# Optimization experiments

Measured on AMD Instinct MI355X. Metric: run time of the kernel, lower is better.

Reference implementation:

```python
import jax, jax.numpy as jnp
import numpy as np

WINDOW_SIZE = 100  # band half-width = WINDOW_SIZE // 2 = 50, inclusive


def setup_inputs() -> dict:
    key = jax.random.key(0)
    kq, kk, kv = jax.random.split(key, 3)
    shape = (2, 8, 4096, 64)  # [B, H, S, D]
    return {
        "query": jax.random.normal(kq, shape, dtype=jnp.float32),
        "key": jax.random.normal(kk, shape, dtype=jnp.float32),
        "value": jax.random.normal(kv, shape, dtype=jnp.float32),
    }


def reference(query, key, value):
    B, H, S, D = query.shape
    half = WINDOW_SIZE // 2
    scale = 1.0 / jnp.sqrt(jnp.asarray(D, dtype=jnp.float32))
    # Full dense scores (faithful to the original module): [B, H, S, S]
    scores = jnp.einsum("bhqd,bhkd->bhqk", query, key) * scale
    # Sliding-window band mask: row i attends to j in [i-half, i+half]
    idx = jnp.arange(S)
    band = jnp.abs(idx[:, None] - idx[None, :]) <= half  # [S, S]
    scores = jnp.where(band[None, None, :, :], scores, -jnp.inf)
    attn = jax.nn.softmax(scores, axis=-1)
    attn = jnp.nan_to_num(attn, nan=0.0)  # matches torch.nan_to_num(w, 0.0)
    return jnp.einsum("bhqk,bhkd->bhqd", attn, value)
```

## Files before the change

### kernel.cpp

```cpp
#include <hip/hip_runtime.h>

#define S_LEN 4096
#define DIM   64
#define HALF  50
#define RB    256
#define WQ    16
#define THREADS 1024
#define KCAP  384
#define SCALE 0.125f

typedef __attribute__((ext_vector_type(8))) short bf16x8;
typedef __attribute__((ext_vector_type(4))) float f32x4;

__device__ __forceinline__ unsigned int bf16_rne(float f) {
    unsigned int u = __float_as_uint(f);
    return (u + 0x7fffu + ((u >> 16) & 1u)) >> 16;
}
__device__ __forceinline__ unsigned int pk2(float lo, float hi) {
    return bf16_rne(lo) | (bf16_rne(hi) << 16);
}

__global__ __launch_bounds__(THREADS)
void lattn_mfma(const float* __restrict__ Q, const float* __restrict__ K,
                const float* __restrict__ V, float* __restrict__ O) {
    __shared__ unsigned short Ks[KCAP * 64];
    __shared__ unsigned short Vs[DIM * KCAP];
    __shared__ unsigned short Ps[16 * 16 * 40];

    const int nwg = gridDim.x;
    const int cpx = nwg >> 3;
    const int bid = blockIdx.x;
    const int logical = (bid & 7) * cpx + (bid >> 3);
    const int bh = logical >> 4;
    const int r0 = (logical & 15) * RB;

    const size_t base = (size_t)bh * (S_LEN * DIM);
    const float* Qg = Q + base;
    const float* Kg = K + base;
    const float* Vg = V + base;
    float*       Og = O + base;

    const int kstart = (r0 >= HALF) ? ((r0 - HALF) & ~31) : 0;
    const int kend   = min(S_LEN, r0 + RB + HALF);
    const int nstep  = (kend - kstart + 31) >> 5;
    const int nkeys  = nstep << 5;

    const int u = threadIdx.x;

    for (int idx = u; idx < (nkeys << 3); idx += THREADS) {
        const int krow = idx >> 3;
        const int oct  = idx & 7;
        const int kg   = kstart + krow;
        unsigned int w0, w1, w2, w3;
        if (kg < kend) {
            const float4 a = *(const float4*)(Kg + (size_t)kg * DIM + oct * 8);
            const float4 b = *(const float4*)(Kg + (size_t)kg * DIM + oct * 8 + 4);
            w0 = pk2(a.x, a.y); w1 = pk2(a.z, a.w);
            w2 = pk2(b.x, b.y); w3 = pk2(b.z, b.w);
        } else { w0 = w1 = w2 = w3 = 0u; }
        *(uint4*)(Ks + krow * 64 + ((oct ^ (krow & 7)) << 3)) = make_uint4(w0, w1, w2, w3);
    }

    for (int idx = u; idx < (nkeys << 2); idx += THREADS) {
        const int kp = idx >> 3;
        const int m  = idx & 7;
        const int d0 = m * 8;
        const int k0 = kp * 2;
        const int kg = kstart + k0;
        unsigned int pw[8];
        if (kg < kend) {
            const float* va = Vg + (size_t)kg * DIM + d0;
            const float* vb = va + DIM;
            float a0[8], a1[8];
            *(float4*)a0 = *(const float4*)va;  *(float4*)(a0 + 4) = *(const float4*)(va + 4);
            *(float4*)a1 = *(const float4*)vb;  *(float4*)(a1 + 4) = *(const float4*)(vb + 4);
            #pragma unroll
            for (int j = 0; j < 8; ++j) pw[j] = pk2(a0[j], a1[j]);
        } else {
            #pragma unroll
            for (int j = 0; j < 8; ++j) pw[j] = 0u;
        }
        #pragma unroll
        for (int j = 0; j < 8; ++j) {
            const int jj = (j + m) & 7;
            const int d  = d0 + jj;
            const int sl = (k0 >> 3) ^ (d & 7);
            *(unsigned int*)(Vs + d * KCAP + sl * 8 + (k0 & 7)) = pw[jj];
        }
    }

    const int lane = u & 63;
    const int wv_  = u >> 6;
    const int g  = lane >> 4;
    const int cc = lane & 15;
    const int qlo = r0 + WQ * wv_;

    bf16x8 qf[2];
    #pragma unroll
    for (int ds = 0; ds < 2; ++ds) {
        const float* src = Qg + (size_t)(qlo + cc) * DIM + ds * 32 + g * 8;
        const float4 a = *(const float4*)src;
        const float4 b = *(const float4*)(src + 4);
        uint4 t = make_uint4(pk2(a.x * SCALE, a.y * SCALE), pk2(a.z * SCALE, a.w * SCALE),
                             pk2(b.x * SCALE, b.y * SCALE), pk2(b.z * SCALE, b.w * SCALE));
        qf[ds] = __builtin_bit_cast(bf16x8, t);
    }

    __syncthreads();

    f32x4 oacc[4] = {};
    float denom = 0.f;

    int lo = (qlo >= HALF) ? (qlo - HALF) : 0;
    lo = max(kstart, lo & ~31);
    const int t0 = (lo - kstart) >> 5;
    const int hi = min(kend, qlo + WQ - 1 + HALF + 1);
    const int t1 = (hi - kstart + 31) >> 5;

    unsigned short* Pw = Ps + wv_ * (16 * 40);

    for (int st = t0; st < t1; ++st) {
        const int kb = st << 5;

        f32x4 sacc[2] = {};
        #pragma unroll
        for (int ds = 0; ds < 2; ++ds) {
            #pragma unroll
            for (int kt = 0; kt < 2; ++kt) {
                const int krow = kb + kt * 16 + cc;
                const int sl   = (ds * 4 + g) ^ (krow & 7);
                const bf16x8 ka = *(const bf16x8*)(Ks + krow * 64 + sl * 8);
                sacc[kt] = __builtin_amdgcn_mfma_f32_16x16x32_bf16(ka, qf[ds], sacc[kt], 0, 0, 0);
            }
        }

        const int q = qlo + cc;
        #pragma unroll
        for (int kt = 0; kt < 2; ++kt) {
            float w4[4];
            const int keyb = kstart + kb + kt * 16 + g * 4;
            #pragma unroll
            for (int r = 0; r < 4; ++r) {
                const int key = keyb + r;
                const float e = __expf(sacc[kt][r]);
                const int dd  = key - q;
                const bool ok = (dd >= -HALF) && (dd <= HALF) && (key < S_LEN);
                w4[r] = ok ? e : 0.f;
                denom += w4[r];
            }
            *(uint2*)(Pw + cc * 40 + kt * 16 + g * 4) = make_uint2(pk2(w4[0], w4[1]), pk2(w4[2], w4[3]));
        }

        const bf16x8 pf = *(const bf16x8*)(Pw + cc * 40 + g * 8);
        #pragma unroll
        for (int dt = 0; dt < 4; ++dt) {
            const int d  = dt * 16 + cc;
            const int sl = ((kb >> 3) + g) ^ (d & 7);
            const bf16x8 vf = *(const bf16x8*)(Vs + d * KCAP + sl * 8);
            oacc[dt] = __builtin_amdgcn_mfma_f32_16x16x32_bf16(vf, pf, oacc[dt], 0, 0, 0);
        }
    }

    denom += __shfl_xor(denom, 16);
    denom += __shfl_xor(denom, 32);
    const float rinv = 1.f / denom;
    float* dst = Og + (size_t)(qlo + cc) * DIM;
    #pragma unroll
    for (int dt = 0; dt < 4; ++dt) {
        const f32x4 o = oacc[dt];
        *(float4*)(dst + dt * 16 + g * 4) =
            make_float4(o[0] * rinv, o[1] * rinv, o[2] * rinv, o[3] * rinv);
    }
}

extern "C" void kernel_launch(void* const* d_in, const int* in_sizes, int n_in,
                              void* d_out, int out_size, void* d_ws, size_t ws_size,
                              hipStream_t stream) {
    const float* q = (const float*)d_in[0];
    const float* k = (const float*)d_in[1];
    const float* v = (const float*)d_in[2];
    float* o = (float*)d_out;
    const int nbh = in_sizes[0] / (S_LEN * DIM);
    dim3 grid((S_LEN / RB) * nbh);
    lattn_mfma<<<grid, THREADS, 0, stream>>>(q, k, v, o);
}
```

Before: 21.84 us.

## Stream K/V into shared memory in chunks, prefetching the next chunk during compute

Replaces the up-front load of all K and V rows into shared memory with three 128-key chunks. The next chunk's global loads are issued into registers before computing on the current chunk, then converted, written to shared memory and followed by a barrier. This is meant to hide global-memory latency behind MFMA work, since each CU runs only one large block. It costs extra barriers and registers, and also clamps the exponent argument to 60 before exp.

```diff
diff --git a/kernel.cpp b/kernel.cpp
--- a/kernel.cpp
+++ b/kernel.cpp
@@ -7,6 +7,8 @@
 #define WQ    16
 #define THREADS 1024
 #define KCAP  384
+#define CHUNK 128
+#define NCH   3
 #define SCALE 0.125f
 
 typedef __attribute__((ext_vector_type(8))) short bf16x8;
@@ -42,51 +44,59 @@
 
     const int kstart = (r0 >= HALF) ? ((r0 - HALF) & ~31) : 0;
     const int kend   = min(S_LEN, r0 + RB + HALF);
-    const int nstep  = (kend - kstart + 31) >> 5;
-    const int nkeys  = nstep << 5;
+    const int nkeys  = ((kend - kstart + 31) >> 5) << 5;
 
     const int u = threadIdx.x;
 
-    for (int idx = u; idx < (nkeys << 3); idx += THREADS) {
-        const int krow = idx >> 3;
-        const int oct  = idx & 7;
-        const int kg   = kstart + krow;
-        unsigned int w0, w1, w2, w3;
+    auto k_load = [&](int c, float4& a, float4& b) {
+        const int kg  = kstart + c * CHUNK + (u >> 3);
+        const int oct = u & 7;
         if (kg < kend) {
-            const float4 a = *(const float4*)(Kg + (size_t)kg * DIM + oct * 8);
-            const float4 b = *(const float4*)(Kg + (size_t)kg * DIM + oct * 8 + 4);
-            w0 = pk2(a.x, a.y); w1 = pk2(a.z, a.w);
-            w2 = pk2(b.x, b.y); w3 = pk2(b.z, b.w);
-        } else { w0 = w1 = w2 = w3 = 0u; }
-        *(uint4*)(Ks + krow * 64 + ((oct ^ (krow & 7)) << 3)) = make_uint4(w0, w1, w2, w3);
-    }
-
-    for (int idx = u; idx < (nkeys << 2); idx += THREADS) {
-        const int kp = idx >> 3;
-        const int m  = idx & 7;
-        const int d0 = m * 8;
-        const int k0 = kp * 2;
-        const int kg = kstart + k0;
-        unsigned int pw[8];
-        if (kg < kend) {
-            const float* va = Vg + (size_t)kg * DIM + d0;
-            const float* vb = va + DIM;
-            float a0[8], a1[8];
-            *(float4*)a0 = *(const float4*)va;  *(float4*)(a0 + 4) = *(const float4*)(va + 4);
-            *(float4*)a1 = *(const float4*)vb;  *(float4*)(a1 + 4) = *(const float4*)(vb + 4);
-            #pragma unroll
-            for (int j = 0; j < 8; ++j) pw[j] = pk2(a0[j], a1[j]);
+            a = *(const float4*)(Kg + (size_t)kg * DIM + oct * 8);
+            b = *(const float4*)(Kg + (size_t)kg * DIM + oct * 8 + 4);
         } else {
-            #pragma unroll
-            for (int j = 0; j < 8; ++j) pw[j] = 0u;
-        }
-        #pragma unroll
-        for (int j = 0; j < 8; ++j) {
-            const int jj = (j + m) & 7;
-            const int d  = d0 + jj;
-            const int sl = (k0 >> 3) ^ (d & 7);
-            *(unsigned int*)(Vs + d * KCAP + sl * 8 + (k0 & 7)) = pw[jj];
-        }
+            a = make_float4(0.f, 0.f, 0.f, 0.f); b = a;
+        }
+    };
+    auto k_write = [&](int c, float4 a, float4 b) {
+        const int krow = c * CHUNK + (u >> 3);
+        const int oct  = u & 7;
+        *(uint4*)(Ks + krow * 64 + ((oct ^ (krow & 7)) << 3)) =
+            make_uint4(pk2(a.x, a.y), pk2(a.z, a.w), pk2(b.x, b.y), pk2(b.z, b.w));
+    };
+    auto v_load = [&](int c, float4* r) {
+        if (u < 512) {
+            const int kg = kstart + c * CHUNK + (u >> 3) * 2;
+            const int d0 = (u & 7) * 8;
+            if (kg < kend) {
+                const float* va = Vg + (size_t)kg * DIM + d0;
+                r[0] = *(const float4*)va;       r[1] = *(const float4*)(va + 4);
+                r[2] = *(const float4*)(va + DIM); r[3] = *(const float4*)(va + DIM + 4);
+            } else {
+                r[0] = make_float4(0.f, 0.f, 0.f, 0.f); r[1] = r[0]; r[2] = r[0]; r[3] = r[0];
+            }
+        }
+    };
+    auto v_write = [&](int c, const float4* r) {
+        if (u < 512) {
+            const int k0 = c * CHUNK + (u >> 3) * 2;
+            const int m  = u & 7;
+            const float* a0 = (const float*)r;
+            const float* a1 = (const float*)(r + 2);
+            #pragma unroll
+            for (int j = 0; j < 8; ++j) {
+                const int jj = (j + m) & 7;
+                const int d  = m * 8 + jj;
+                const int sl = (k0 >> 3) ^ (d & 7);
+                *(unsigned int*)(Vs + d * KCAP + sl * 8 + (k0 & 7)) = pk2(a0[jj], a1[jj]);
+            }
+        }
+    };
+
+    {
+        float4 ka, kb, vr[4];
+        k_load(0, ka, kb); v_load(0, vr);
+        k_write(0, ka, kb); v_write(0, vr);
     }
 
     const int lane = u & 63;
@@ -119,45 +129,60 @@
 
     unsigned short* Pw = Ps + wv_ * (16 * 40);
 
-    for (int st = t0; st < t1; ++st) {
-        const int kb = st << 5;
-
-        f32x4 sacc[2] = {};
-        #pragma unroll
-        for (int ds = 0; ds < 2; ++ds) {
+    for (int c = 0; c < NCH; ++c) {
+        float4 ka, kb, vr[4];
+        const bool more = (c + 1 < NCH) && ((c + 1) * CHUNK < nkeys);
+        if (more) { k_load(c + 1, ka, kb); v_load(c + 1, vr); }
+
+        const int sa = max(t0, c * 4);
+        const int sb = min(t1, c * 4 + 4);
+        for (int st = sa; st < sb; ++st) {
+            const int kb32 = st << 5;
+
+            f32x4 sacc[2] = {};
+            #pragma unroll
+            for (int ds = 0; ds < 2; ++ds) {
+                #pragma unroll
+                for (int kt = 0; kt < 2; ++kt) {
+                    const int krow = kb32 + kt * 16 + cc;
+                    const int sl   = (ds * 4 + g) ^ (krow & 7);
+                    const bf16x8 kfr = *(const bf16x8*)(Ks + krow * 64 + sl * 8);
+                    sacc[kt] = __builtin_amdgcn_mfma_f32_16x16x32_bf16(kfr, qf[ds], sacc[kt], 0, 0, 0);
+                }
+            }
+
+            const int q = qlo + cc;
             #pragma unroll
             for (int kt = 0; kt < 2; ++kt) {
-                const int krow = kb + kt * 16 + cc;
-                const int sl   = (ds * 4 + g) ^ (krow & 7);
-                const bf16x8 ka = *(const bf16x8*)(Ks + krow * 64 + sl * 8);
-                sacc[kt] = __builtin_amdgcn_mfma_f32_16x16x32_bf16(ka, qf[ds], sacc[kt], 0, 0, 0);
-            }
-        }
-
-        const int q = qlo + cc;
-        #pragma unroll
-        for (int kt = 0; kt < 2; ++kt) {
-            float w4[4];
-            const int keyb = kstart + kb + kt * 16 + g * 4;
-            #pragma unroll
-            for (int r = 0; r < 4; ++r) {
-                const int key = keyb + r;
-                const float e = __expf(sacc[kt][r]);
-                const int dd  = key - q;
-                const bool ok = (dd >= -HALF) && (dd <= HALF) && (key < S_LEN);
-                w4[r] = ok ? e : 0.f;
-                denom += w4[r];
-            }
-            *(uint2*)(Pw + cc * 40 + kt * 16 + g * 4) = make_uint2(pk2(w4[0], w4[1]), pk2(w4[2], w4[3]));
-        }
-
-        const bf16x8 pf = *(const bf16x8*)(Pw + cc * 40 + g * 8);
-        #pragma unroll
-        for (int dt = 0; dt < 4; ++dt) {
-            const int d  = dt * 16 + cc;
-            const int sl = ((kb >> 3) + g) ^ (d & 7);
-            const bf16x8 vf = *(const bf16x8*)(Vs + d * KCAP + sl * 8);
-            oacc[dt] = __builtin_amdgcn_mfma_f32_16x16x32_bf16(vf, pf, oacc[dt], 0, 0, 0);
+                float w4[4];
+                const int keyb = kstart + kb32 + kt * 16 + g * 4;
+                #pragma unroll
+                for (int r = 0; r < 4; ++r) {
+                    const int key = keyb + r;
+                    const float e = __expf(fminf(sacc[kt][r], 60.f));
+                    const int dd  = key - q;
+                    const bool ok = (dd >= -HALF) && (dd <= HALF) && (key < S_LEN);
+                    w4[r] = ok ? e : 0.f;
+                    denom += w4[r];
+                }
+                *(uint2*)(Pw + cc * 40 + kt * 16 + g * 4) =
+                    make_uint2(pk2(w4[0], w4[1]), pk2(w4[2], w4[3]));
+            }
+
+            const bf16x8 pf = *(const bf16x8*)(Pw + cc * 40 + g * 8);
+            #pragma unroll
+            for (int dt = 0; dt < 4; ++dt) {
+                const int d  = dt * 16 + cc;
+                const int sl = ((kb32 >> 3) + g) ^ (d & 7);
+                const bf16x8 vf = *(const bf16x8*)(Vs + d * KCAP + sl * 8);
+                oacc[dt] = __builtin_amdgcn_mfma_f32_16x16x32_bf16(vf, pf, oacc[dt], 0, 0, 0);
+            }
+        }
+
+        if (more) {
+            k_write(c + 1, ka, kb);
+            v_write(c + 1, vr);
+            __syncthreads();
         }
     }
 
```

After: 30.67 us. 1.4x slower.

## Load K directly from global per wave and overlap QK^T with V staging

Applied to the files above, without the earlier changes.

Removes the shared-memory K staging buffer: each wave reads its K rows straight from global memory, converts them to bf16 in registers and computes scores and probabilities for up to NT key tiles before the block barrier. This lets the QK^T/softmax work overlap with the cooperative V-to-LDS transpose, and the smaller LDS footprint plus launch_bounds(…,4) aims to raise occupancy. The V layout gets an extra XOR swizzle term to cut bank conflicts, and exp inputs are clamped at 60. The cost is redundant global K reads across waves (served mostly by cache) and extra registers to hold the buffered P fragments.

```diff
diff --git a/kernel.cpp b/kernel.cpp
--- a/kernel.cpp
+++ b/kernel.cpp
@@ -7,6 +7,7 @@
 #define WQ    16
 #define THREADS 1024
 #define KCAP  384
+#define NT    5
 #define SCALE 0.125f
 
 typedef __attribute__((ext_vector_type(8))) short bf16x8;
@@ -19,11 +20,14 @@
 __device__ __forceinline__ unsigned int pk2(float lo, float hi) {
     return bf16_rne(lo) | (bf16_rne(hi) << 16);
 }
+__device__ __forceinline__ bf16x8 cvt8(float4 a, float4 b) {
+    uint4 t = make_uint4(pk2(a.x, a.y), pk2(a.z, a.w), pk2(b.x, b.y), pk2(b.z, b.w));
+    return __builtin_bit_cast(bf16x8, t);
+}
 
-__global__ __launch_bounds__(THREADS)
+__global__ __launch_bounds__(THREADS, 4)
 void lattn_mfma(const float* __restrict__ Q, const float* __restrict__ K,
                 const float* __restrict__ V, float* __restrict__ O) {
-    __shared__ unsigned short Ks[KCAP * 64];
     __shared__ unsigned short Vs[DIM * KCAP];
     __shared__ unsigned short Ps[16 * 16 * 40];
 
@@ -42,24 +46,14 @@
 
     const int kstart = (r0 >= HALF) ? ((r0 - HALF) & ~31) : 0;
     const int kend   = min(S_LEN, r0 + RB + HALF);
-    const int nstep  = (kend - kstart + 31) >> 5;
-    const int nkeys  = nstep << 5;
+    const int nkeys  = ((kend - kstart + 31) >> 5) << 5;
 
     const int u = threadIdx.x;
-
-    for (int idx = u; idx < (nkeys << 3); idx += THREADS) {
-        const int krow = idx >> 3;
-        const int oct  = idx & 7;
-        const int kg   = kstart + krow;
-        unsigned int w0, w1, w2, w3;
-        if (kg < kend) {
-            const float4 a = *(const float4*)(Kg + (size_t)kg * DIM + oct * 8);
-            const float4 b = *(const float4*)(Kg + (size_t)kg * DIM + oct * 8 + 4);
-            w0 = pk2(a.x, a.y); w1 = pk2(a.z, a.w);
-            w2 = pk2(b.x, b.y); w3 = pk2(b.z, b.w);
-        } else { w0 = w1 = w2 = w3 = 0u; }
-        *(uint4*)(Ks + krow * 64 + ((oct ^ (krow & 7)) << 3)) = make_uint4(w0, w1, w2, w3);
-    }
+    const int lane = u & 63;
+    const int wv_  = u >> 6;
+    const int g  = lane >> 4;
+    const int cc = lane & 15;
+    const int qlo = r0 + WQ * wv_;
 
     for (int idx = u; idx < (nkeys << 2); idx += THREADS) {
         const int kp = idx >> 3;
@@ -67,49 +61,33 @@
         const int d0 = m * 8;
         const int k0 = kp * 2;
         const int kg = kstart + k0;
-        unsigned int pw[8];
+        float a0[8], a1[8];
         if (kg < kend) {
             const float* va = Vg + (size_t)kg * DIM + d0;
-            const float* vb = va + DIM;
-            float a0[8], a1[8];
-            *(float4*)a0 = *(const float4*)va;  *(float4*)(a0 + 4) = *(const float4*)(va + 4);
-            *(float4*)a1 = *(const float4*)vb;  *(float4*)(a1 + 4) = *(const float4*)(vb + 4);
-            #pragma unroll
-            for (int j = 0; j < 8; ++j) pw[j] = pk2(a0[j], a1[j]);
+            *(float4*)a0 = *(const float4*)va;        *(float4*)(a0 + 4) = *(const float4*)(va + 4);
+            *(float4*)a1 = *(const float4*)(va + DIM); *(float4*)(a1 + 4) = *(const float4*)(va + DIM + 4);
         } else {
             #pragma unroll
-            for (int j = 0; j < 8; ++j) pw[j] = 0u;
+            for (int j = 0; j < 8; ++j) { a0[j] = 0.f; a1[j] = 0.f; }
         }
         #pragma unroll
         for (int j = 0; j < 8; ++j) {
-            const int jj = (j + m) & 7;
-            const int d  = d0 + jj;
-            const int sl = (k0 >> 3) ^ (d & 7);
-            *(unsigned int*)(Vs + d * KCAP + sl * 8 + (k0 & 7)) = pw[jj];
+            const int d  = d0 + j;
+            const int sl = (k0 >> 3) ^ (d & 7) ^ ((d >> 3) & 7);
+            *(unsigned int*)(Vs + d * KCAP + sl * 8 + (k0 & 7)) = pk2(a0[j], a1[j]);
         }
     }
-
-    const int lane = u & 63;
-    const int wv_  = u >> 6;
-    const int g  = lane >> 4;
-    const int cc = lane & 15;
-    const int qlo = r0 + WQ * wv_;
 
     bf16x8 qf[2];
     #pragma unroll
     for (int ds = 0; ds < 2; ++ds) {
         const float* src = Qg + (size_t)(qlo + cc) * DIM + ds * 32 + g * 8;
-        const float4 a = *(const float4*)src;
-        const float4 b = *(const float4*)(src + 4);
-        uint4 t = make_uint4(pk2(a.x * SCALE, a.y * SCALE), pk2(a.z * SCALE, a.w * SCALE),
-                             pk2(b.x * SCALE, b.y * SCALE), pk2(b.z * SCALE, b.w * SCALE));
-        qf[ds] = __builtin_bit_cast(bf16x8, t);
+        float4 a = *(const float4*)src;
+        float4 b = *(const float4*)(src + 4);
+        a.x *= SCALE; a.y *= SCALE; a.z *= SCALE; a.w *= SCALE;
+        b.x *= SCALE; b.y *= SCALE; b.z *= SCALE; b.w *= SCALE;
+        qf[ds] = cvt8(a, b);
     }
-
-    __syncthreads();
-
-    f32x4 oacc[4] = {};
-    float denom = 0.f;
 
     int lo = (qlo >= HALF) ? (qlo - HALF) : 0;
     lo = max(kstart, lo & ~31);
@@ -118,46 +96,78 @@
     const int t1 = (hi - kstart + 31) >> 5;
 
     unsigned short* Pw = Ps + wv_ * (16 * 40);
+    float denom = 0.f;
+    bf16x8 pfr[NT];
 
-    for (int st = t0; st < t1; ++st) {
-        const int kb = st << 5;
+    #pragma unroll
+    for (int i = 0; i < NT; ++i) {
+        const int st = t0 + i;
+        if (st < t1) {
+            const int kb32 = st << 5;
 
-        f32x4 sacc[2] = {};
-        #pragma unroll
-        for (int ds = 0; ds < 2; ++ds) {
+            bf16x8 ka[2][2];
             #pragma unroll
             for (int kt = 0; kt < 2; ++kt) {
-                const int krow = kb + kt * 16 + cc;
-                const int sl   = (ds * 4 + g) ^ (krow & 7);
-                const bf16x8 ka = *(const bf16x8*)(Ks + krow * 64 + sl * 8);
-                sacc[kt] = __builtin_amdgcn_mfma_f32_16x16x32_bf16(ka, qf[ds], sacc[kt], 0, 0, 0);
+                const int krow = kstart + kb32 + kt * 16 + cc;
+                if (krow < kend) {
+                    const float* kp_ = Kg + (size_t)krow * DIM + g * 8;
+                    const float4 a0 = *(const float4*)kp_;
+                    const float4 a1 = *(const float4*)(kp_ + 4);
+                    const float4 b0 = *(const float4*)(kp_ + 32);
+                    const float4 b1 = *(const float4*)(kp_ + 36);
+                    ka[0][kt] = cvt8(a0, a1);
+                    ka[1][kt] = cvt8(b0, b1);
+                } else {
+                    uint4 z = make_uint4(0u, 0u, 0u, 0u);
+                    ka[0][kt] = __builtin_bit_cast(bf16x8, z);
+                    ka[1][kt] = __builtin_bit_cast(bf16x8, z);
+                }
             }
+
+            f32x4 sacc[2] = {};
+            #pragma unroll
+            for (int ds = 0; ds < 2; ++ds) {
+                #pragma unroll
+                for (int kt = 0; kt < 2; ++kt)
+                    sacc[kt] = __builtin_amdgcn_mfma_f32_16x16x32_bf16(ka[ds][kt], qf[ds], sacc[kt], 0, 0, 0);
+            }
+
+            const int q = qlo + cc;
+            #pragma unroll
+            for (int kt = 0; kt < 2; ++kt) {
+                float w4[4];
+                const int keyb = kstart + kb32 + kt * 16 + g * 4;
+                #pragma unroll
+                for (int r = 0; r < 4; ++r) {
+                    const int key = keyb + r;
+                    const float e = __expf(fminf(sacc[kt][r], 60.f));
+                    const int dd  = key - q;
+                    const bool ok = (dd >= -HALF) && (dd <= HALF) && (key < S_LEN);
+                    w4[r] = ok ? e : 0.f;
+                    denom += w4[r];
+                }
+                *(uint2*)(Pw + cc * 40 + kt * 16 + g * 4) =
+                    make_uint2(pk2(w4[0], w4[1]), pk2(w4[2], w4[3]));
+            }
+            pfr[i] = *(const bf16x8*)(Pw + cc * 40 + g * 8);
         }
+    }
 
-        const int q = qlo + cc;
-        #pragma unroll
-        for (int kt = 0; kt < 2; ++kt) {
-            float w4[4];
-            const int keyb = kstart + kb + kt * 16 + g * 4;
+    __syncthreads();
+
+    f32x4 oacc[4] = {};
+    #pragma unroll
+    for (int i = 0; i < NT; ++i) {
+        const int st = t0 + i;
+        if (st < t1) {
+            const int kb32 = st << 5;
             #pragma unroll
-            for (int r = 0; r < 4; ++r) {
-                const int key = keyb + r;
-                const float e = __expf(sacc[kt][r]);
-                const int dd  = key - q;
-                const bool ok = (dd >= -HALF) && (dd <= HALF) && (key < S_LEN);
-                w4[r] = ok ? e : 0.f;
-                denom += w4[r];
+            for (int dt = 0; dt < 4; ++dt) {
+                const int d  = dt * 16 + cc;
+                const int sl = ((kb32 >> 3) + g) ^ (d & 7) ^ ((d >> 3) & 7);
+                const bf16x8 vf = *(const bf16x8*)(Vs + d * KCAP + sl * 8);
+                oacc[dt] = __builtin_amdgcn_mfma_f32_16x16x32_bf16(vf, pfr[i], oacc[dt], 0, 0, 0);
             }
-            *(uint2*)(Pw + cc * 40 + kt * 16 + g * 4) = make_uint2(pk2(w4[0], w4[1]), pk2(w4[2], w4[3]));
-        }
-
-        const bf16x8 pf = *(const bf16x8*)(Pw + cc * 40 + g * 8);
-        #pragma unroll
-        for (int dt = 0; dt < 4; ++dt) {
-            const int d  = dt * 16 + cc;
-            const int sl = ((kb >> 3) + g) ^ (d & 7);
-            const bf16x8 vf = *(const bf16x8*)(Vs + d * KCAP + sl * 8);
-            oacc[dt] = __builtin_amdgcn_mfma_f32_16x16x32_bf16(vf, pf, oacc[dt], 0, 0, 0);
         }
     }
 
```

After: 34.55 us. 1.58x slower.
